# Optimization experiments

Measured on AMD Instinct MI355X. Metric: run time of the kernel, lower is better.

The kernel has to match this reference:

```python
import jax, jax.numpy as jnp
import numpy as np

N_NODES = 50000
N_EDGES = 800000
IN_CH = 128
HID = 256
N_GRAPHS = 512


def setup_inputs() -> dict:
    key = jax.random.key(0)
    ks = jax.random.split(key, 10)
    x = jax.random.normal(ks[0], (N_NODES, IN_CH), dtype=jnp.float32)
    edge_index = jax.random.randint(ks[1], (2, N_EDGES), 0, N_NODES, dtype=jnp.int32)
    batch = jnp.sort(jax.random.randint(ks[2], (N_NODES,), 0, N_GRAPHS, dtype=jnp.int32))
    # GCNConv params (glorot-ish init)
    W0 = jax.random.normal(ks[3], (IN_CH, HID), dtype=jnp.float32) / np.sqrt(IN_CH)
    b0 = jnp.zeros((HID,), dtype=jnp.float32)
    W1 = jax.random.normal(ks[4], (HID, HID), dtype=jnp.float32) / np.sqrt(HID)
    b1 = jnp.zeros((HID,), dtype=jnp.float32)
    W2 = jax.random.normal(ks[5], (HID, HID), dtype=jnp.float32) / np.sqrt(HID)
    b2 = jnp.zeros((HID,), dtype=jnp.float32)
    return {"x": x, "W0": W0, "b0": b0, "W1": W1, "b1": b1, "W2": W2, "b2": b2,
            "edge_index": edge_index, "batch": batch}


def _gcn_norm(edge_index, num_nodes):
    # PyG gcn_norm with add_self_loops=True: A_hat = A + I, norm = D^-1/2 A_hat D^-1/2
    src, dst = edge_index[0], edge_index[1]
    loop = jnp.arange(num_nodes, dtype=src.dtype)
    src = jnp.concatenate([src, loop])
    dst = jnp.concatenate([dst, loop])
    deg = jax.ops.segment_sum(jnp.ones_like(dst, dtype=jnp.float32), dst,
                              num_segments=num_nodes)
    dinv = jnp.where(deg > 0, jax.lax.rsqrt(deg), 0.0)
    norm = dinv[src] * dinv[dst]  # [E + N]
    return src, dst, norm


def _gcn_conv(x, W, b, src, dst, norm, num_nodes):
    h = x @ W                                  # [N, out]
    msg = norm[:, None] * h[src]               # gather + scale, [E+N, out]
    out = jax.ops.segment_sum(msg, dst, num_segments=num_nodes)  # scatter-add
    return out + b


def reference(x, W0, b0, W1, b1, W2, b2, edge_index, batch):
    n = x.shape[0]
    src, dst, norm = _gcn_norm(edge_index, n)  # normalization is layer-independent
    h = jax.nn.relu(_gcn_conv(x, W0, b0, src, dst, norm, n))
    h = jax.nn.relu(_gcn_conv(h, W1, b1, src, dst, norm, n))
    h = jax.nn.relu(_gcn_conv(h, W2, b2, src, dst, norm, n))
    # global_add_pool: segment-sum node features by graph id
    return jax.ops.segment_sum(h, batch, num_segments=N_GRAPHS)
```

## Files before the change

### kernel.cpp

```cpp
#include <hip/hip_runtime.h>
#include <hip/hip_fp16.h>

constexpr int NN  = 50000;
constexpr int NE  = 800000;
constexpr int CIN = 128;
constexpr int CH  = 256;
constexpr int NG  = 512;

typedef unsigned short ushort_t;
typedef unsigned int uint_t;
typedef unsigned char uchar_t;
typedef __attribute__((ext_vector_type(2))) float f32x2_t;
typedef __attribute__((ext_vector_type(2))) uint_t u32x2_t;

static __device__ __forceinline__ ushort_t f2bf(float f) {
    uint_t u = __float_as_uint(f);
    u += 0x7fffu + ((u >> 16) & 1u);
    return (ushort_t)(u >> 16);
}

static __device__ __forceinline__ float h16tof(uint_t bits) {
    return __half2float(__ushort_as_half((unsigned short)bits));
}

__global__ void conv_x_kernel(const float4* __restrict__ x, ushort4* __restrict__ xb, int n4) {
    int i = blockIdx.x * blockDim.x + threadIdx.x;
    if (i >= n4) return;
    float4 v = x[i];
    ushort4 o;
    o.x = f2bf(v.x); o.y = f2bf(v.y); o.z = f2bf(v.z); o.w = f2bf(v.w);
    xb[i] = o;
}

__global__ void conv_wt3_kernel(const float* __restrict__ W0, const float* __restrict__ W1,
                                const float* __restrict__ W2, ushort_t* __restrict__ W0t,
                                ushort_t* __restrict__ W1t, ushort_t* __restrict__ W2t) {
    int i = blockIdx.x * blockDim.x + threadIdx.x;
    if (i < 32768) {
        int k = i >> 8, n = i & 255;
        W0t[n * 128 + k] = f2bf(W0[i]);
    } else if (i < 98304) {
        int j = i - 32768;
        int k = j >> 8, n = j & 255;
        W1t[n * 256 + k] = f2bf(W1[j]);
    } else if (i < 163840) {
        int j = i - 98304;
        int k = j >> 8, n = j & 255;
        W2t[n * 256 + k] = f2bf(W2[j]);
    }
}

__global__ void count_kernel(const int* __restrict__ dst, int* __restrict__ cnt, int E) {
    int e = blockIdx.x * blockDim.x + threadIdx.x;
    if (e < E) atomicAdd(&cnt[dst[e]], 1);
}

__global__ __launch_bounds__(256) void scan_bsum_kernel(const int* __restrict__ cnt,
                                                        int* __restrict__ bsum, int n) {
    int i = blockIdx.x * 256 + threadIdx.x;
    int v = (i < n) ? ((cnt[i] + 7) & ~7) : 0;
    #pragma unroll
    for (int off = 32; off >= 1; off >>= 1) v += __shfl_xor(v, off, 64);
    __shared__ int ws[4];
    if ((threadIdx.x & 63) == 0) ws[threadIdx.x >> 6] = v;
    __syncthreads();
    if (threadIdx.x == 0) bsum[blockIdx.x] = ws[0] + ws[1] + ws[2] + ws[3];
}

__global__ __launch_bounds__(256) void scan_boff_kernel(int* __restrict__ bsum, int nb) {
    int tid = threadIdx.x, lane = tid & 63, wid = tid >> 6;
    int v = (tid < nb) ? bsum[tid] : 0;
    int s = v;
    #pragma unroll
    for (int off = 1; off < 64; off <<= 1) {
        int t = __shfl_up(s, off, 64);
        if (lane >= off) s += t;
    }
    __shared__ int wsum[4];
    if (lane == 63) wsum[wid] = s;
    __syncthreads();
    int wadd = 0;
    #pragma unroll
    for (int w = 0; w < 4; w++) if (w < wid) wadd += wsum[w];
    if (tid < nb) bsum[tid] = wadd + s - v;
}

__global__ __launch_bounds__(256) void scan_final_kernel(const int* __restrict__ cnt,
                                                         const int* __restrict__ boff,
                                                         int* __restrict__ rowptr,
                                                         float* __restrict__ dinv, int n) {
    int tid = threadIdx.x, lane = tid & 63, wid = tid >> 6;
    int i = blockIdx.x * 256 + tid;
    int c = (i < n) ? cnt[i] : 0;
    int v = (c + 7) & ~7;
    int s = v;
    #pragma unroll
    for (int off = 1; off < 64; off <<= 1) {
        int t = __shfl_up(s, off, 64);
        if (lane >= off) s += t;
    }
    __shared__ int wsum[4];
    if (lane == 63) wsum[wid] = s;
    __syncthreads();
    int wadd = boff[blockIdx.x];
    #pragma unroll
    for (int w = 0; w < 4; w++) if (w < wid) wadd += wsum[w];
    if (i < n) {
        rowptr[i] = wadd + s - v;
        dinv[i]   = rsqrtf((float)c + 1.0f);
        if (i == n - 1) rowptr[n] = wadd + s;
    }
}

__global__ void scatter_kernel(const int* __restrict__ src, const int* __restrict__ dst,
                               const int* __restrict__ rowptr, int* __restrict__ cursor,
                               const float* __restrict__ dinv, uint_t* __restrict__ epack, int E) {
    int e = blockIdx.x * blockDim.x + threadIdx.x;
    if (e >= E) return;
    int d = dst[e];
    int s = src[e];
    int p = rowptr[d] + atomicAdd(&cursor[d], 1);
    uint_t hb = (uint_t)__half_as_ushort(__float2half(dinv[s]));
    epack[p] = (uint_t)s | (hb << 16);
}

template <int C, int MODE>
__global__ __launch_bounds__(256) void node_agg_kernel(
    const ushort_t* __restrict__ h, const int* __restrict__ rowptr,
    const int* __restrict__ degc, const uint_t* __restrict__ epack,
    const float* __restrict__ dinv, const float* __restrict__ bias,
    const int* __restrict__ batch, void* __restrict__ out_v, int n) {
    constexpr int V = C / 64;
    int wave = threadIdx.x >> 6;
    int lane = threadIdx.x & 63;
    int d = blockIdx.x * 4 + wave;
    if (d >= n) return;

    int beg = __builtin_amdgcn_readfirstlane(rowptr[d]);
    int deg = __builtin_amdgcn_readfirstlane(degc[d]);
    const uint_t* hu = (const uint_t*)h;

    float acc[V] = {};
    const uint4* ep4 = (const uint4*)(epack + beg);
    uint4 ea, eb, na, nb;
    if (deg > 0) { ea = ep4[0]; eb = ep4[1]; }

    for (int e = 0; e < deg; e += 8) {
        int blk = e >> 3;
        if (e + 8 < deg) { na = ep4[blk * 2 + 2]; nb = ep4[blk * 2 + 3]; }
        uint_t eps[8] = {ea.x, ea.y, ea.z, ea.w, eb.x, eb.y, eb.z, eb.w};
        int   srcs[8];
        float wts[8];
        #pragma unroll
        for (int u = 0; u < 8; u++) {
            bool a = (e + u) < deg;
            srcs[u] = a ? (int)(eps[u] & 0xffffu) : d;
            wts[u]  = a ? h16tof(eps[u] >> 16) : 0.0f;
        }
        if constexpr (V == 4) {
            uint_t ra[8], rb[8];
            #pragma unroll
            for (int u = 0; u < 8; u++) {
                const uint_t* row = hu + (size_t)__builtin_amdgcn_readfirstlane(srcs[u]) * (C / 2);
                ra[u] = row[lane];
                rb[u] = row[64 + lane];
            }
            #pragma unroll
            for (int u = 0; u < 8; u++) {
                float w = wts[u];
                acc[0] += w * __uint_as_float(ra[u] << 16);
                acc[1] += w * __uint_as_float(ra[u] & 0xffff0000u);
                acc[2] += w * __uint_as_float(rb[u] << 16);
                acc[3] += w * __uint_as_float(rb[u] & 0xffff0000u);
            }
        } else {
            uint_t rv[8];
            #pragma unroll
            for (int u = 0; u < 8; u++) {
                const uint_t* row = hu + (size_t)__builtin_amdgcn_readfirstlane(srcs[u]) * (C / 2);
                rv[u] = row[lane];
            }
            #pragma unroll
            for (int u = 0; u < 8; u++) {
                float w = wts[u];
                acc[0] += w * __uint_as_float(rv[u] << 16);
                acc[1] += w * __uint_as_float(rv[u] & 0xffff0000u);
            }
        }
        ea = na; eb = nb;
    }

    float dd = dinv[d];
    float self[V];
    {
        const uint_t* row = hu + (size_t)d * (C / 2);
        uint_t sa = row[lane];
        self[0] = __uint_as_float(sa << 16);
        self[1] = __uint_as_float(sa & 0xffff0000u);
        if constexpr (V == 4) {
            uint_t sb = row[64 + lane];
            self[2] = __uint_as_float(sb << 16);
            self[3] = __uint_as_float(sb & 0xffff0000u);
        }
    }

    float r[V];
    if constexpr (MODE >= 1) {
        float2 bA = *(const float2*)(bias + 2 * lane);
        r[0] = fmaxf(dd * acc[0] + dd * dd * self[0] + bA.x, 0.0f);
        r[1] = fmaxf(dd * acc[1] + dd * dd * self[1] + bA.y, 0.0f);
        if constexpr (V == 4) {
            float2 bB = *(const float2*)(bias + 128 + 2 * lane);
            r[2] = fmaxf(dd * acc[2] + dd * dd * self[2] + bB.x, 0.0f);
            r[3] = fmaxf(dd * acc[3] + dd * dd * self[3] + bB.y, 0.0f);
        }
    } else {
        #pragma unroll
        for (int i = 0; i < V; i++)
            r[i] = dd * acc[i] + dd * dd * self[i];
    }

    if constexpr (MODE == 2) {
        float* o = (float*)out_v + (size_t)batch[d] * C;
        atomicAdd(o + 2 * lane, r[0]);
        atomicAdd(o + 2 * lane + 1, r[1]);
        if constexpr (V == 4) {
            atomicAdd(o + 128 + 2 * lane, r[2]);
            atomicAdd(o + 128 + 2 * lane + 1, r[3]);
        }
    } else {
        uint_t* o = (uint_t*)((ushort_t*)out_v + (size_t)d * C);
        __builtin_nontemporal_store((uint_t)f2bf(r[0]) | ((uint_t)f2bf(r[1]) << 16), &o[lane]);
        if constexpr (V == 4)
            __builtin_nontemporal_store((uint_t)f2bf(r[2]) | ((uint_t)f2bf(r[3]) << 16), &o[64 + lane]);
    }
}

template <int MODE>
__global__ __launch_bounds__(256) void node_agg_fp8_kernel(
    const uchar_t* __restrict__ h8, const int* __restrict__ rowptr,
    const int* __restrict__ degc, const uint_t* __restrict__ epack,
    const float* __restrict__ dinv, const float* __restrict__ bias,
    const int* __restrict__ batch, void* __restrict__ out_v, int n) {
    int wave = threadIdx.x >> 6;
    int lane = threadIdx.x & 63;
    int d = blockIdx.x * 4 + wave;
    if (d >= n) return;

    int beg = __builtin_amdgcn_readfirstlane(rowptr[d]);
    int deg = __builtin_amdgcn_readfirstlane(degc[d]);
    const uint_t* hu = (const uint_t*)h8;

    float a0 = 0.0f, a1 = 0.0f, a2 = 0.0f, a3 = 0.0f;
    const uint4* ep4 = (const uint4*)(epack + beg);
    uint4 ea, eb, na, nb;
    if (deg > 0) { ea = ep4[0]; eb = ep4[1]; }

    for (int e = 0; e < deg; e += 8) {
        int blk = e >> 3;
        if (e + 8 < deg) { na = ep4[blk * 2 + 2]; nb = ep4[blk * 2 + 3]; }
        uint_t eps[8] = {ea.x, ea.y, ea.z, ea.w, eb.x, eb.y, eb.z, eb.w};
        int   srcs[8];
        float wts[8];
        #pragma unroll
        for (int u = 0; u < 8; u++) {
            bool a = (e + u) < deg;
            srcs[u] = a ? (int)(eps[u] & 0xffffu) : d;
            wts[u]  = a ? h16tof(eps[u] >> 16) : 0.0f;
        }
        uint_t rv[8];
        #pragma unroll
        for (int u = 0; u < 8; u++)
            rv[u] = hu[(size_t)__builtin_amdgcn_readfirstlane(srcs[u]) * 64 + lane];
        #pragma unroll
        for (int u = 0; u < 8; u++) {
            float w = wts[u];
            f32x2_t lo = __builtin_amdgcn_cvt_pk_f32_fp8(rv[u], false);
            f32x2_t hi = __builtin_amdgcn_cvt_pk_f32_fp8(rv[u], true);
            a0 += w * lo.x;
            a1 += w * lo.y;
            a2 += w * hi.x;
            a3 += w * hi.y;
        }
        ea = na; eb = nb;
    }

    float dd = dinv[d];
    uint_t sv = hu[(size_t)d * 64 + lane];
    f32x2_t slo = __builtin_amdgcn_cvt_pk_f32_fp8(sv, false);
    f32x2_t shi = __builtin_amdgcn_cvt_pk_f32_fp8(sv, true);

    float4 b4 = *(const float4*)(bias + 4 * lane);
    float dd2 = dd * dd;
    float r0 = fmaxf(dd * a0 + dd2 * slo.x + b4.x, 0.0f);
    float r1 = fmaxf(dd * a1 + dd2 * slo.y + b4.y, 0.0f);
    float r2 = fmaxf(dd * a2 + dd2 * shi.x + b4.z, 0.0f);
    float r3 = fmaxf(dd * a3 + dd2 * shi.y + b4.w, 0.0f);

    if constexpr (MODE == 2) {
        float* o = (float*)out_v + (size_t)batch[d] * CH + 4 * lane;
        atomicAdd(o + 0, r0);
        atomicAdd(o + 1, r1);
        atomicAdd(o + 2, r2);
        atomicAdd(o + 3, r3);
    } else {
        u32x2_t st;
        st.x = (uint_t)f2bf(r0) | ((uint_t)f2bf(r1) << 16);
        st.y = (uint_t)f2bf(r2) | ((uint_t)f2bf(r3) << 16);
        u32x2_t* o = (u32x2_t*)((ushort_t*)out_v + (size_t)d * CH) + lane;
        __builtin_nontemporal_store(st, o);
    }
}

typedef __attribute__((ext_vector_type(8))) short bf16x8;
typedef __attribute__((ext_vector_type(4))) float f32x4;

template <int MODE, int F8OUT>
__global__ __launch_bounds__(256) void gemm_bf16_kernel(
    const ushort_t* __restrict__ A, const ushort_t* __restrict__ Wt,
    const float* __restrict__ bias, void* __restrict__ Cv, int M, int K) {
    __shared__ ushort_t As[128][40];
    __shared__ ushort_t Bs[128][40];
    int tid = threadIdx.x;
    int row0 = blockIdx.x * 128, col0 = blockIdx.y * 128;
    int lr = tid >> 2, lq = tid & 3;
    int lane = tid & 63, wv = tid >> 6;
    int wr = (wv >> 1) * 64, wc = (wv & 1) * 64;
    int r16 = lane & 15, quad = lane >> 4;

    f32x4 acc[4][4] = {};

    for (int k0 = 0; k0 < K; k0 += 32) {
        {
            int gr0 = row0 + lr, gr1 = row0 + lr + 64;
            uint4 a0 = make_uint4(0, 0, 0, 0), a1 = make_uint4(0, 0, 0, 0);
            if (gr0 < M) a0 = *(const uint4*)(A + (size_t)gr0 * K + k0 + lq * 8);
            if (gr1 < M) a1 = *(const uint4*)(A + (size_t)gr1 * K + k0 + lq * 8);
            *(uint4*)&As[lr][lq * 8]      = a0;
            *(uint4*)&As[lr + 64][lq * 8] = a1;
            uint4 b0 = *(const uint4*)(Wt + (size_t)(col0 + lr) * K + k0 + lq * 8);
            uint4 b1 = *(const uint4*)(Wt + (size_t)(col0 + lr + 64) * K + k0 + lq * 8);
            *(uint4*)&Bs[lr][lq * 8]      = b0;
            *(uint4*)&Bs[lr + 64][lq * 8] = b1;
        }
        __syncthreads();
        bf16x8 af[4], bfr[4];
        #pragma unroll
        for (int i = 0; i < 4; i++) af[i]  = *(const bf16x8*)&As[wr + i * 16 + r16][quad * 8];
        #pragma unroll
        for (int j = 0; j < 4; j++) bfr[j] = *(const bf16x8*)&Bs[wc + j * 16 + r16][quad * 8];
        #pragma unroll
        for (int i = 0; i < 4; i++)
            #pragma unroll
            for (int j = 0; j < 4; j++)
                acc[i][j] = __builtin_amdgcn_mfma_f32_16x16x32_bf16(af[i], bfr[j], acc[i][j], 0, 0, 0);
        __syncthreads();
    }

    #pragma unroll
    for (int j = 0; j < 4; j++) {
        int colc = col0 + wc + j * 16 + r16;
        float bval = (MODE == 1) ? bias[colc] : 0.0f;
        #pragma unroll
        for (int i = 0; i < 4; i++) {
            #pragma unroll
            for (int r = 0; r < 4; r++) {
                int row = row0 + wr + i * 16 + quad * 4 + r;
                if (row < M) {
                    float v = acc[i][j][r];
                    if (MODE == 1) v = fmaxf(v + bval, 0.0f);
                    if constexpr (F8OUT) {
                        uint_t pk = __builtin_amdgcn_cvt_pk_fp8_f32(v, v, 0u, false);
                        ((uchar_t*)Cv)[(size_t)row * 256 + colc] = (uchar_t)(pk & 0xffu);
                    } else {
                        ((ushort_t*)Cv)[(size_t)row * 256 + colc] = f2bf(v);
                    }
                }
            }
        }
    }
}

extern "C" void kernel_launch(void* const* d_in, const int* in_sizes, int n_in,
                              void* d_out, int out_size, void* d_ws, size_t ws_size,
                              hipStream_t stream) {
    const float* x   = (const float*)d_in[0];
    const float* W0  = (const float*)d_in[1];
    const float* b0  = (const float*)d_in[2];
    const float* W1  = (const float*)d_in[3];
    const float* b1  = (const float*)d_in[4];
    const float* W2  = (const float*)d_in[5];
    const float* b2  = (const float*)d_in[6];
    const int*   ei  = (const int*)d_in[7];
    const int*   src = ei;
    const int*   dst = ei + NE;
    const int*   batch = (const int*)d_in[8];
    float* out = (float*)d_out;

    char* ws = (char*)d_ws;
    ushort_t* P1  = (ushort_t*)ws;
    ushort_t* G0  = (ushort_t*)(ws + 25600000ull);
    uchar_t*  F8  = (uchar_t*) (ws + 38400000ull);
    ushort_t* xbf = (ushort_t*)(ws + 51200000ull);
    ushort_t* W0t = (ushort_t*)(ws + 64000000ull);
    ushort_t* W1t = (ushort_t*)(ws + 64065536ull);
    ushort_t* W2t = (ushort_t*)(ws + 64196608ull);
    float*    dinv   = (float*)(ws + 64327680ull);
    int*      rowptr = (int*)  (ws + 64527680ull);
    int*      cnt    = (int*)  (ws + 64727808ull);
    uint_t*   epack  = (uint_t*)(ws + 64927808ull);
    int*      bsum   = (int*)  (ws + 71327808ull);
    int*      cursor = (int*)ws;

    const int scanBlocks = (NN + 255) / 256;
    const int nodeBlocks = (NN + 3) / 4;
    const dim3 ggrid((NN + 127) / 128, 2);

    conv_x_kernel<<<(NN * CIN / 4 + 255) / 256, 256, 0, stream>>>((const float4*)x, (ushort4*)xbf, NN * CIN / 4);
    conv_wt3_kernel<<<640, 256, 0, stream>>>(W0, W1, W2, W0t, W1t, W2t);

    hipMemsetAsync(cnt, 0, (size_t)NN * 4, stream);
    count_kernel<<<(NE + 255) / 256, 256, 0, stream>>>(dst, cnt, NE);
    scan_bsum_kernel<<<scanBlocks, 256, 0, stream>>>(cnt, bsum, NN);
    scan_boff_kernel<<<1, 256, 0, stream>>>(bsum, scanBlocks);
    scan_final_kernel<<<scanBlocks, 256, 0, stream>>>(cnt, bsum, rowptr, dinv, NN);
    hipMemsetAsync(cursor, 0, (size_t)NN * 4, stream);
    scatter_kernel<<<(NE + 255) / 256, 256, 0, stream>>>(src, dst, rowptr, cursor, dinv, epack, NE);

    node_agg_kernel<CIN, 0><<<nodeBlocks, 256, 0, stream>>>(xbf, rowptr, cnt, epack, dinv, nullptr, nullptr, G0, NN);
    gemm_bf16_kernel<1, 0><<<ggrid, 256, 0, stream>>>(G0, W0t, b0, P1, NN, CIN);

    gemm_bf16_kernel<0, 1><<<ggrid, 256, 0, stream>>>(P1, W1t, nullptr, F8, NN, CH);
    node_agg_fp8_kernel<1><<<nodeBlocks, 256, 0, stream>>>(F8, rowptr, cnt, epack, dinv, b1, nullptr, P1, NN);

    gemm_bf16_kernel<0, 1><<<ggrid, 256, 0, stream>>>(P1, W2t, nullptr, F8, NN, CH);
    hipMemsetAsync(out, 0, (size_t)NG * CH * 4, stream);
    node_agg_fp8_kernel<2><<<nodeBlocks, 256, 0, stream>>>(F8, rowptr, cnt, epack, dinv, b2, batch, out, NN);
}
```

Before: 489.3 us.

## Stage fp8 GEMM output through LDS for coalesced stores; drop nontemporal stores

The fp8-output GEMM epilogue now writes converted bytes into a shared-memory tile that aliases the A/B staging buffers, then stores whole rows to global memory as 16-byte vectors instead of scattered single-byte writes. Nontemporal stores in the node-aggregation kernels are replaced with ordinary stores, so the bf16 outputs can stay in cache for the GEMM that reads them next. A READ2 variant of the fp8 aggregation, reading two 16-bit halves per lane with a matching output layout, is enabled only for the final pooling layer. The costs are an extra barrier and LDS round trip in the epilogue, plus narrower gathers in the last layer.

```diff
diff --git a/kernel.cpp b/kernel.cpp
--- a/kernel.cpp
+++ b/kernel.cpp
@@ -230,13 +230,13 @@
         }
     } else {
         uint_t* o = (uint_t*)((ushort_t*)out_v + (size_t)d * C);
-        __builtin_nontemporal_store((uint_t)f2bf(r[0]) | ((uint_t)f2bf(r[1]) << 16), &o[lane]);
+        o[lane] = (uint_t)f2bf(r[0]) | ((uint_t)f2bf(r[1]) << 16);
         if constexpr (V == 4)
-            __builtin_nontemporal_store((uint_t)f2bf(r[2]) | ((uint_t)f2bf(r[3]) << 16), &o[64 + lane]);
-    }
-}
-
-template <int MODE>
+            o[64 + lane] = (uint_t)f2bf(r[2]) | ((uint_t)f2bf(r[3]) << 16);
+    }
+}
+
+template <int MODE, int READ2>
 __global__ __launch_bounds__(256) void node_agg_fp8_kernel(
     const uchar_t* __restrict__ h8, const int* __restrict__ rowptr,
     const int* __restrict__ degc, const uint_t* __restrict__ epack,
@@ -249,7 +249,6 @@
 
     int beg = __builtin_amdgcn_readfirstlane(rowptr[d]);
     int deg = __builtin_amdgcn_readfirstlane(degc[d]);
-    const uint_t* hu = (const uint_t*)h8;
 
     float a0 = 0.0f, a1 = 0.0f, a2 = 0.0f, a3 = 0.0f;
     const uint4* ep4 = (const uint4*)(epack + beg);
@@ -268,47 +267,90 @@
             srcs[u] = a ? (int)(eps[u] & 0xffffu) : d;
             wts[u]  = a ? h16tof(eps[u] >> 16) : 0.0f;
         }
-        uint_t rv[8];
-        #pragma unroll
-        for (int u = 0; u < 8; u++)
-            rv[u] = hu[(size_t)__builtin_amdgcn_readfirstlane(srcs[u]) * 64 + lane];
-        #pragma unroll
-        for (int u = 0; u < 8; u++) {
-            float w = wts[u];
-            f32x2_t lo = __builtin_amdgcn_cvt_pk_f32_fp8(rv[u], false);
-            f32x2_t hi = __builtin_amdgcn_cvt_pk_f32_fp8(rv[u], true);
-            a0 += w * lo.x;
-            a1 += w * lo.y;
-            a2 += w * hi.x;
-            a3 += w * hi.y;
+        if constexpr (READ2) {
+            uint_t ra[8], rb[8];
+            #pragma unroll
+            for (int u = 0; u < 8; u++) {
+                const ushort_t* row = (const ushort_t*)h8 + (size_t)__builtin_amdgcn_readfirstlane(srcs[u]) * 128;
+                ra[u] = row[lane];
+                rb[u] = row[64 + lane];
+            }
+            #pragma unroll
+            for (int u = 0; u < 8; u++) {
+                float w = wts[u];
+                f32x2_t lo = __builtin_amdgcn_cvt_pk_f32_fp8(ra[u], false);
+                f32x2_t hi = __builtin_amdgcn_cvt_pk_f32_fp8(rb[u], false);
+                a0 += w * lo.x;
+                a1 += w * lo.y;
+                a2 += w * hi.x;
+                a3 += w * hi.y;
+            }
+        } else {
+            const uint_t* hu = (const uint_t*)h8;
+            uint_t rv[8];
+            #pragma unroll
+            for (int u = 0; u < 8; u++)
+                rv[u] = hu[(size_t)__builtin_amdgcn_readfirstlane(srcs[u]) * 64 + lane];
+            #pragma unroll
+            for (int u = 0; u < 8; u++) {
+                float w = wts[u];
+                f32x2_t lo = __builtin_amdgcn_cvt_pk_f32_fp8(rv[u], false);
+                f32x2_t hi = __builtin_amdgcn_cvt_pk_f32_fp8(rv[u], true);
+                a0 += w * lo.x;
+                a1 += w * lo.y;
+                a2 += w * hi.x;
+                a3 += w * hi.y;
+            }
         }
         ea = na; eb = nb;
     }
 
     float dd = dinv[d];
-    uint_t sv = hu[(size_t)d * 64 + lane];
-    f32x2_t slo = __builtin_amdgcn_cvt_pk_f32_fp8(sv, false);
-    f32x2_t shi = __builtin_amdgcn_cvt_pk_f32_fp8(sv, true);
-
-    float4 b4 = *(const float4*)(bias + 4 * lane);
     float dd2 = dd * dd;
-    float r0 = fmaxf(dd * a0 + dd2 * slo.x + b4.x, 0.0f);
-    float r1 = fmaxf(dd * a1 + dd2 * slo.y + b4.y, 0.0f);
-    float r2 = fmaxf(dd * a2 + dd2 * shi.x + b4.z, 0.0f);
-    float r3 = fmaxf(dd * a3 + dd2 * shi.y + b4.w, 0.0f);
-
-    if constexpr (MODE == 2) {
-        float* o = (float*)out_v + (size_t)batch[d] * CH + 4 * lane;
-        atomicAdd(o + 0, r0);
-        atomicAdd(o + 1, r1);
-        atomicAdd(o + 2, r2);
-        atomicAdd(o + 3, r3);
+
+    if constexpr (READ2) {
+        const ushort_t* srow = (const ushort_t*)h8 + (size_t)d * 128;
+        f32x2_t slo = __builtin_amdgcn_cvt_pk_f32_fp8((uint_t)srow[lane], false);
+        f32x2_t shi = __builtin_amdgcn_cvt_pk_f32_fp8((uint_t)srow[64 + lane], false);
+        float2 bA = *(const float2*)(bias + 2 * lane);
+        float2 bB = *(const float2*)(bias + 128 + 2 * lane);
+        float r0 = fmaxf(dd * a0 + dd2 * slo.x + bA.x, 0.0f);
+        float r1 = fmaxf(dd * a1 + dd2 * slo.y + bA.y, 0.0f);
+        float r2 = fmaxf(dd * a2 + dd2 * shi.x + bB.x, 0.0f);
+        float r3 = fmaxf(dd * a3 + dd2 * shi.y + bB.y, 0.0f);
+        if constexpr (MODE == 2) {
+            float* o = (float*)out_v + (size_t)batch[d] * CH;
+            atomicAdd(o + 2 * lane, r0);
+            atomicAdd(o + 2 * lane + 1, r1);
+            atomicAdd(o + 128 + 2 * lane, r2);
+            atomicAdd(o + 128 + 2 * lane + 1, r3);
+        } else {
+            uint_t* o = (uint_t*)((ushort_t*)out_v + (size_t)d * CH);
+            o[lane]      = (uint_t)f2bf(r0) | ((uint_t)f2bf(r1) << 16);
+            o[64 + lane] = (uint_t)f2bf(r2) | ((uint_t)f2bf(r3) << 16);
+        }
     } else {
-        u32x2_t st;
-        st.x = (uint_t)f2bf(r0) | ((uint_t)f2bf(r1) << 16);
-        st.y = (uint_t)f2bf(r2) | ((uint_t)f2bf(r3) << 16);
-        u32x2_t* o = (u32x2_t*)((ushort_t*)out_v + (size_t)d * CH) + lane;
-        __builtin_nontemporal_store(st, o);
+        const uint_t* hu = (const uint_t*)h8;
+        uint_t sv = hu[(size_t)d * 64 + lane];
+        f32x2_t slo = __builtin_amdgcn_cvt_pk_f32_fp8(sv, false);
+        f32x2_t shi = __builtin_amdgcn_cvt_pk_f32_fp8(sv, true);
+        float4 b4 = *(const float4*)(bias + 4 * lane);
+        float r0 = fmaxf(dd * a0 + dd2 * slo.x + b4.x, 0.0f);
+        float r1 = fmaxf(dd * a1 + dd2 * slo.y + b4.y, 0.0f);
+        float r2 = fmaxf(dd * a2 + dd2 * shi.x + b4.z, 0.0f);
+        float r3 = fmaxf(dd * a3 + dd2 * shi.y + b4.w, 0.0f);
+        if constexpr (MODE == 2) {
+            float* o = (float*)out_v + (size_t)batch[d] * CH + 4 * lane;
+            atomicAdd(o + 0, r0);
+            atomicAdd(o + 1, r1);
+            atomicAdd(o + 2, r2);
+            atomicAdd(o + 3, r3);
+        } else {
+            u32x2_t st;
+            st.x = (uint_t)f2bf(r0) | ((uint_t)f2bf(r1) << 16);
+            st.y = (uint_t)f2bf(r2) | ((uint_t)f2bf(r3) << 16);
+            *((u32x2_t*)((ushort_t*)out_v + (size_t)d * CH) + lane) = st;
+        }
     }
 }
 
@@ -319,8 +361,10 @@
 __global__ __launch_bounds__(256) void gemm_bf16_kernel(
     const ushort_t* __restrict__ A, const ushort_t* __restrict__ Wt,
     const float* __restrict__ bias, void* __restrict__ Cv, int M, int K) {
-    __shared__ ushort_t As[128][40];
-    __shared__ ushort_t Bs[128][40];
+    __shared__ union alignas(16) {
+        ushort_t ab[2][128][40];
+        uchar_t  f8[128][128];
+    } smem;
     int tid = threadIdx.x;
     int row0 = blockIdx.x * 128, col0 = blockIdx.y * 128;
     int lr = tid >> 2, lq = tid & 3;
@@ -336,19 +380,19 @@
             uint4 a0 = make_uint4(0, 0, 0, 0), a1 = make_uint4(0, 0, 0, 0);
             if (gr0 < M) a0 = *(const uint4*)(A + (size_t)gr0 * K + k0 + lq * 8);
             if (gr1 < M) a1 = *(const uint4*)(A + (size_t)gr1 * K + k0 + lq * 8);
-            *(uint4*)&As[lr][lq * 8]      = a0;
-            *(uint4*)&As[lr + 64][lq * 8] = a1;
+            *(uint4*)&smem.ab[0][lr][lq * 8]      = a0;
+            *(uint4*)&smem.ab[0][lr + 64][lq * 8] = a1;
             uint4 b0 = *(const uint4*)(Wt + (size_t)(col0 + lr) * K + k0 + lq * 8);
             uint4 b1 = *(const uint4*)(Wt + (size_t)(col0 + lr + 64) * K + k0 + lq * 8);
-            *(uint4*)&Bs[lr][lq * 8]      = b0;
-            *(uint4*)&Bs[lr + 64][lq * 8] = b1;
+            *(uint4*)&smem.ab[1][lr][lq * 8]      = b0;
+            *(uint4*)&smem.ab[1][lr + 64][lq * 8] = b1;
         }
         __syncthreads();
         bf16x8 af[4], bfr[4];
         #pragma unroll
-        for (int i = 0; i < 4; i++) af[i]  = *(const bf16x8*)&As[wr + i * 16 + r16][quad * 8];
-        #pragma unroll
-        for (int j = 0; j < 4; j++) bfr[j] = *(const bf16x8*)&Bs[wc + j * 16 + r16][quad * 8];
+        for (int i = 0; i < 4; i++) af[i]  = *(const bf16x8*)&smem.ab[0][wr + i * 16 + r16][quad * 8];
+        #pragma unroll
+        for (int j = 0; j < 4; j++) bfr[j] = *(const bf16x8*)&smem.ab[1][wc + j * 16 + r16][quad * 8];
         #pragma unroll
         for (int i = 0; i < 4; i++)
             #pragma unroll
@@ -357,22 +401,43 @@
         __syncthreads();
     }
 
-    #pragma unroll
-    for (int j = 0; j < 4; j++) {
-        int colc = col0 + wc + j * 16 + r16;
-        float bval = (MODE == 1) ? bias[colc] : 0.0f;
-        #pragma unroll
-        for (int i = 0; i < 4; i++) {
-            #pragma unroll
-            for (int r = 0; r < 4; r++) {
-                int row = row0 + wr + i * 16 + quad * 4 + r;
-                if (row < M) {
+    if constexpr (F8OUT) {
+        #pragma unroll
+        for (int j = 0; j < 4; j++) {
+            int colt = wc + j * 16 + r16;
+            #pragma unroll
+            for (int i = 0; i < 4; i++) {
+                #pragma unroll
+                for (int r = 0; r < 4; r++) {
                     float v = acc[i][j][r];
-                    if (MODE == 1) v = fmaxf(v + bval, 0.0f);
-                    if constexpr (F8OUT) {
-                        uint_t pk = __builtin_amdgcn_cvt_pk_fp8_f32(v, v, 0u, false);
-                        ((uchar_t*)Cv)[(size_t)row * 256 + colc] = (uchar_t)(pk & 0xffu);
-                    } else {
+                    uint_t pk = __builtin_amdgcn_cvt_pk_fp8_f32(v, v, 0u, false);
+                    smem.f8[wr + i * 16 + quad * 4 + r][colt] = (uchar_t)(pk & 0xffu);
+                }
+            }
+        }
+        __syncthreads();
+        uchar_t* C8 = (uchar_t*)Cv;
+        #pragma unroll
+        for (int k = 0; k < 4; k++) {
+            int idx = k * 256 + tid;
+            int r = idx >> 3, coff = (idx & 7) * 16;
+            if (row0 + r < M)
+                *(uint4*)(C8 + (size_t)(row0 + r) * 256 + col0 + coff) =
+                    *(const uint4*)&smem.f8[r][coff];
+        }
+    } else {
+        #pragma unroll
+        for (int j = 0; j < 4; j++) {
+            int colc = col0 + wc + j * 16 + r16;
+            float bval = (MODE == 1) ? bias[colc] : 0.0f;
+            #pragma unroll
+            for (int i = 0; i < 4; i++) {
+                #pragma unroll
+                for (int r = 0; r < 4; r++) {
+                    int row = row0 + wr + i * 16 + quad * 4 + r;
+                    if (row < M) {
+                        float v = acc[i][j][r];
+                        if (MODE == 1) v = fmaxf(v + bval, 0.0f);
                         ((ushort_t*)Cv)[(size_t)row * 256 + colc] = f2bf(v);
                     }
                 }
@@ -431,9 +496,9 @@
     gemm_bf16_kernel<1, 0><<<ggrid, 256, 0, stream>>>(G0, W0t, b0, P1, NN, CIN);
 
     gemm_bf16_kernel<0, 1><<<ggrid, 256, 0, stream>>>(P1, W1t, nullptr, F8, NN, CH);
-    node_agg_fp8_kernel<1><<<nodeBlocks, 256, 0, stream>>>(F8, rowptr, cnt, epack, dinv, b1, nullptr, P1, NN);
+    node_agg_fp8_kernel<1, 0><<<nodeBlocks, 256, 0, stream>>>(F8, rowptr, cnt, epack, dinv, b1, nullptr, P1, NN);
 
     gemm_bf16_kernel<0, 1><<<ggrid, 256, 0, stream>>>(P1, W2t, nullptr, F8, NN, CH);
     hipMemsetAsync(out, 0, (size_t)NG * CH * 4, stream);
-    node_agg_fp8_kernel<2><<<nodeBlocks, 256, 0, stream>>>(F8, rowptr, cnt, epack, dinv, b2, batch, out, NN);
-}
+    node_agg_fp8_kernel<2, 1><<<nodeBlocks, 256, 0, stream>>>(F8, rowptr, cnt, epack, dinv, b2, batch, out, NN);
+}
```

Measured after the change: 397.3 us. 18.8% less time.

## Widen edge batches to 16 and stage FP8 GEMM output through LDS

Applied to the files above, without the earlier changes.

Row padding in the CSR grows from 8 to 16 edges, and both aggregation kernels now handle 16 neighbor gathers per iteration. This puts more independent loads in flight to hide gather latency. The FP8 GEMM epilogue now writes its tile into shared memory and then stores 16-byte coalesced rows, replacing the scattered single-byte global stores. Nontemporal stores become plain stores and the first-layer aggregation becomes a dedicated 128-channel kernel. The trade-offs are higher register pressure, more padded edge slots to load, and an extra barrier in the GEMM.

```diff
diff --git a/kernel.cpp b/kernel.cpp
--- a/kernel.cpp
+++ b/kernel.cpp
@@ -58,7 +58,7 @@
 __global__ __launch_bounds__(256) void scan_bsum_kernel(const int* __restrict__ cnt,
                                                         int* __restrict__ bsum, int n) {
     int i = blockIdx.x * 256 + threadIdx.x;
-    int v = (i < n) ? ((cnt[i] + 7) & ~7) : 0;
+    int v = (i < n) ? ((cnt[i] + 15) & ~15) : 0;
     #pragma unroll
     for (int off = 32; off >= 1; off >>= 1) v += __shfl_xor(v, off, 64);
     __shared__ int ws[4];
@@ -92,7 +92,7 @@
     int tid = threadIdx.x, lane = tid & 63, wid = tid >> 6;
     int i = blockIdx.x * 256 + tid;
     int c = (i < n) ? cnt[i] : 0;
-    int v = (c + 7) & ~7;
+    int v = (c + 15) & ~15;
     int s = v;
     #pragma unroll
     for (int off = 1; off < 64; off <<= 1) {
@@ -124,13 +124,10 @@
     epack[p] = (uint_t)s | (hb << 16);
 }
 
-template <int C, int MODE>
-__global__ __launch_bounds__(256) void node_agg_kernel(
+__global__ __launch_bounds__(256) void node_agg_bf16_kernel(
     const ushort_t* __restrict__ h, const int* __restrict__ rowptr,
     const int* __restrict__ degc, const uint_t* __restrict__ epack,
-    const float* __restrict__ dinv, const float* __restrict__ bias,
-    const int* __restrict__ batch, void* __restrict__ out_v, int n) {
-    constexpr int V = C / 64;
+    const float* __restrict__ dinv, ushort_t* __restrict__ outp, int n) {
     int wave = threadIdx.x >> 6;
     int lane = threadIdx.x & 63;
     int d = blockIdx.x * 4 + wave;
@@ -140,100 +137,48 @@
     int deg = __builtin_amdgcn_readfirstlane(degc[d]);
     const uint_t* hu = (const uint_t*)h;
 
-    float acc[V] = {};
+    float a0 = 0.0f, a1 = 0.0f;
     const uint4* ep4 = (const uint4*)(epack + beg);
-    uint4 ea, eb, na, nb;
-    if (deg > 0) { ea = ep4[0]; eb = ep4[1]; }
-
-    for (int e = 0; e < deg; e += 8) {
-        int blk = e >> 3;
-        if (e + 8 < deg) { na = ep4[blk * 2 + 2]; nb = ep4[blk * 2 + 3]; }
-        uint_t eps[8] = {ea.x, ea.y, ea.z, ea.w, eb.x, eb.y, eb.z, eb.w};
-        int   srcs[8];
-        float wts[8];
-        #pragma unroll
-        for (int u = 0; u < 8; u++) {
+    uint4 e0, e1, e2, e3;
+    if (deg > 0) { e0 = ep4[0]; e1 = ep4[1]; e2 = ep4[2]; e3 = ep4[3]; }
+    uint4 n0 = e0, n1 = e1, n2 = e2, n3 = e3;
+
+    for (int e = 0; e < deg; e += 16) {
+        int blk = e >> 4;
+        if (e + 16 < deg) {
+            n0 = ep4[blk * 4 + 4]; n1 = ep4[blk * 4 + 5];
+            n2 = ep4[blk * 4 + 6]; n3 = ep4[blk * 4 + 7];
+        }
+        uint_t eps[16] = {e0.x, e0.y, e0.z, e0.w, e1.x, e1.y, e1.z, e1.w,
+                          e2.x, e2.y, e2.z, e2.w, e3.x, e3.y, e3.z, e3.w};
+        int   srcs[16];
+        float wts[16];
+        #pragma unroll
+        for (int u = 0; u < 16; u++) {
             bool a = (e + u) < deg;
             srcs[u] = a ? (int)(eps[u] & 0xffffu) : d;
             wts[u]  = a ? h16tof(eps[u] >> 16) : 0.0f;
         }
-        if constexpr (V == 4) {
-            uint_t ra[8], rb[8];
-            #pragma unroll
-            for (int u = 0; u < 8; u++) {
-                const uint_t* row = hu + (size_t)__builtin_amdgcn_readfirstlane(srcs[u]) * (C / 2);
-                ra[u] = row[lane];
-                rb[u] = row[64 + lane];
-            }
-            #pragma unroll
-            for (int u = 0; u < 8; u++) {
-                float w = wts[u];
-                acc[0] += w * __uint_as_float(ra[u] << 16);
-                acc[1] += w * __uint_as_float(ra[u] & 0xffff0000u);
-                acc[2] += w * __uint_as_float(rb[u] << 16);
-                acc[3] += w * __uint_as_float(rb[u] & 0xffff0000u);
-            }
-        } else {
-            uint_t rv[8];
-            #pragma unroll
-            for (int u = 0; u < 8; u++) {
-                const uint_t* row = hu + (size_t)__builtin_amdgcn_readfirstlane(srcs[u]) * (C / 2);
-                rv[u] = row[lane];
-            }
-            #pragma unroll
-            for (int u = 0; u < 8; u++) {
-                float w = wts[u];
-                acc[0] += w * __uint_as_float(rv[u] << 16);
-                acc[1] += w * __uint_as_float(rv[u] & 0xffff0000u);
-            }
-        }
-        ea = na; eb = nb;
+        uint_t rv[16];
+        #pragma unroll
+        for (int u = 0; u < 16; u++)
+            rv[u] = hu[(size_t)__builtin_amdgcn_readfirstlane(srcs[u]) * 64 + lane];
+        #pragma unroll
+        for (int u = 0; u < 16; u++) {
+            float w = wts[u];
+            a0 += w * __uint_as_float(rv[u] << 16);
+            a1 += w * __uint_as_float(rv[u] & 0xffff0000u);
+        }
+        e0 = n0; e1 = n1; e2 = n2; e3 = n3;
     }
 
     float dd = dinv[d];
-    float self[V];
-    {
-        const uint_t* row = hu + (size_t)d * (C / 2);
-        uint_t sa = row[lane];
-        self[0] = __uint_as_float(sa << 16);
-        self[1] = __uint_as_float(sa & 0xffff0000u);
-        if constexpr (V == 4) {
-            uint_t sb = row[64 + lane];
-            self[2] = __uint_as_float(sb << 16);
-            self[3] = __uint_as_float(sb & 0xffff0000u);
-        }
-    }
-
-    float r[V];
-    if constexpr (MODE >= 1) {
-        float2 bA = *(const float2*)(bias + 2 * lane);
-        r[0] = fmaxf(dd * acc[0] + dd * dd * self[0] + bA.x, 0.0f);
-        r[1] = fmaxf(dd * acc[1] + dd * dd * self[1] + bA.y, 0.0f);
-        if constexpr (V == 4) {
-            float2 bB = *(const float2*)(bias + 128 + 2 * lane);
-            r[2] = fmaxf(dd * acc[2] + dd * dd * self[2] + bB.x, 0.0f);
-            r[3] = fmaxf(dd * acc[3] + dd * dd * self[3] + bB.y, 0.0f);
-        }
-    } else {
-        #pragma unroll
-        for (int i = 0; i < V; i++)
-            r[i] = dd * acc[i] + dd * dd * self[i];
-    }
-
-    if constexpr (MODE == 2) {
-        float* o = (float*)out_v + (size_t)batch[d] * C;
-        atomicAdd(o + 2 * lane, r[0]);
-        atomicAdd(o + 2 * lane + 1, r[1]);
-        if constexpr (V == 4) {
-            atomicAdd(o + 128 + 2 * lane, r[2]);
-            atomicAdd(o + 128 + 2 * lane + 1, r[3]);
-        }
-    } else {
-        uint_t* o = (uint_t*)((ushort_t*)out_v + (size_t)d * C);
-        __builtin_nontemporal_store((uint_t)f2bf(r[0]) | ((uint_t)f2bf(r[1]) << 16), &o[lane]);
-        if constexpr (V == 4)
-            __builtin_nontemporal_store((uint_t)f2bf(r[2]) | ((uint_t)f2bf(r[3]) << 16), &o[64 + lane]);
-    }
+    uint_t sv = hu[(size_t)d * 64 + lane];
+    float r0 = dd * a0 + dd * dd * __uint_as_float(sv << 16);
+    float r1 = dd * a1 + dd * dd * __uint_as_float(sv & 0xffff0000u);
+
+    uint_t* o = (uint_t*)(outp + (size_t)d * CIN);
+    o[lane] = (uint_t)f2bf(r0) | ((uint_t)f2bf(r1) << 16);
 }
 
 template <int MODE>
@@ -253,27 +198,32 @@
 
     float a0 = 0.0f, a1 = 0.0f, a2 = 0.0f, a3 = 0.0f;
     const uint4* ep4 = (const uint4*)(epack + beg);
-    uint4 ea, eb, na, nb;
-    if (deg > 0) { ea = ep4[0]; eb = ep4[1]; }
-
-    for (int e = 0; e < deg; e += 8) {
-        int blk = e >> 3;
-        if (e + 8 < deg) { na = ep4[blk * 2 + 2]; nb = ep4[blk * 2 + 3]; }
-        uint_t eps[8] = {ea.x, ea.y, ea.z, ea.w, eb.x, eb.y, eb.z, eb.w};
-        int   srcs[8];
-        float wts[8];
-        #pragma unroll
-        for (int u = 0; u < 8; u++) {
+    uint4 e0, e1, e2, e3;
+    if (deg > 0) { e0 = ep4[0]; e1 = ep4[1]; e2 = ep4[2]; e3 = ep4[3]; }
+    uint4 n0 = e0, n1 = e1, n2 = e2, n3 = e3;
+
+    for (int e = 0; e < deg; e += 16) {
+        int blk = e >> 4;
+        if (e + 16 < deg) {
+            n0 = ep4[blk * 4 + 4]; n1 = ep4[blk * 4 + 5];
+            n2 = ep4[blk * 4 + 6]; n3 = ep4[blk * 4 + 7];
+        }
+        uint_t eps[16] = {e0.x, e0.y, e0.z, e0.w, e1.x, e1.y, e1.z, e1.w,
+                          e2.x, e2.y, e2.z, e2.w, e3.x, e3.y, e3.z, e3.w};
+        int   srcs[16];
+        float wts[16];
+        #pragma unroll
+        for (int u = 0; u < 16; u++) {
             bool a = (e + u) < deg;
             srcs[u] = a ? (int)(eps[u] & 0xffffu) : d;
             wts[u]  = a ? h16tof(eps[u] >> 16) : 0.0f;
         }
-        uint_t rv[8];
-        #pragma unroll
-        for (int u = 0; u < 8; u++)
+        uint_t rv[16];
+        #pragma unroll
+        for (int u = 0; u < 16; u++)
             rv[u] = hu[(size_t)__builtin_amdgcn_readfirstlane(srcs[u]) * 64 + lane];
         #pragma unroll
-        for (int u = 0; u < 8; u++) {
+        for (int u = 0; u < 16; u++) {
             float w = wts[u];
             f32x2_t lo = __builtin_amdgcn_cvt_pk_f32_fp8(rv[u], false);
             f32x2_t hi = __builtin_amdgcn_cvt_pk_f32_fp8(rv[u], true);
@@ -282,16 +232,16 @@
             a2 += w * hi.x;
             a3 += w * hi.y;
         }
-        ea = na; eb = nb;
+        e0 = n0; e1 = n1; e2 = n2; e3 = n3;
     }
 
     float dd = dinv[d];
+    float dd2 = dd * dd;
     uint_t sv = hu[(size_t)d * 64 + lane];
     f32x2_t slo = __builtin_amdgcn_cvt_pk_f32_fp8(sv, false);
     f32x2_t shi = __builtin_amdgcn_cvt_pk_f32_fp8(sv, true);
 
     float4 b4 = *(const float4*)(bias + 4 * lane);
-    float dd2 = dd * dd;
     float r0 = fmaxf(dd * a0 + dd2 * slo.x + b4.x, 0.0f);
     float r1 = fmaxf(dd * a1 + dd2 * slo.y + b4.y, 0.0f);
     float r2 = fmaxf(dd * a2 + dd2 * shi.x + b4.z, 0.0f);
@@ -307,8 +257,7 @@
         u32x2_t st;
         st.x = (uint_t)f2bf(r0) | ((uint_t)f2bf(r1) << 16);
         st.y = (uint_t)f2bf(r2) | ((uint_t)f2bf(r3) << 16);
-        u32x2_t* o = (u32x2_t*)((ushort_t*)out_v + (size_t)d * CH) + lane;
-        __builtin_nontemporal_store(st, o);
+        *((u32x2_t*)((ushort_t*)out_v + (size_t)d * CH) + lane) = st;
     }
 }
 
@@ -319,8 +268,10 @@
 __global__ __launch_bounds__(256) void gemm_bf16_kernel(
     const ushort_t* __restrict__ A, const ushort_t* __restrict__ Wt,
     const float* __restrict__ bias, void* __restrict__ Cv, int M, int K) {
-    __shared__ ushort_t As[128][40];
-    __shared__ ushort_t Bs[128][40];
+    __shared__ union alignas(16) {
+        ushort_t ab[2][128][40];
+        uchar_t  f8[128][128];
+    } smem;
     int tid = threadIdx.x;
     int row0 = blockIdx.x * 128, col0 = blockIdx.y * 128;
     int lr = tid >> 2, lq = tid & 3;
@@ -336,19 +287,19 @@
             uint4 a0 = make_uint4(0, 0, 0, 0), a1 = make_uint4(0, 0, 0, 0);
             if (gr0 < M) a0 = *(const uint4*)(A + (size_t)gr0 * K + k0 + lq * 8);
             if (gr1 < M) a1 = *(const uint4*)(A + (size_t)gr1 * K + k0 + lq * 8);
-            *(uint4*)&As[lr][lq * 8]      = a0;
-            *(uint4*)&As[lr + 64][lq * 8] = a1;
+            *(uint4*)&smem.ab[0][lr][lq * 8]      = a0;
+            *(uint4*)&smem.ab[0][lr + 64][lq * 8] = a1;
             uint4 b0 = *(const uint4*)(Wt + (size_t)(col0 + lr) * K + k0 + lq * 8);
             uint4 b1 = *(const uint4*)(Wt + (size_t)(col0 + lr + 64) * K + k0 + lq * 8);
-            *(uint4*)&Bs[lr][lq * 8]      = b0;
-            *(uint4*)&Bs[lr + 64][lq * 8] = b1;
+            *(uint4*)&smem.ab[1][lr][lq * 8]      = b0;
+            *(uint4*)&smem.ab[1][lr + 64][lq * 8] = b1;
         }
         __syncthreads();
         bf16x8 af[4], bfr[4];
         #pragma unroll
-        for (int i = 0; i < 4; i++) af[i]  = *(const bf16x8*)&As[wr + i * 16 + r16][quad * 8];
-        #pragma unroll
-        for (int j = 0; j < 4; j++) bfr[j] = *(const bf16x8*)&Bs[wc + j * 16 + r16][quad * 8];
+        for (int i = 0; i < 4; i++) af[i]  = *(const bf16x8*)&smem.ab[0][wr + i * 16 + r16][quad * 8];
+        #pragma unroll
+        for (int j = 0; j < 4; j++) bfr[j] = *(const bf16x8*)&smem.ab[1][wc + j * 16 + r16][quad * 8];
         #pragma unroll
         for (int i = 0; i < 4; i++)
             #pragma unroll
@@ -357,22 +308,43 @@
         __syncthreads();
     }
 
-    #pragma unroll
-    for (int j = 0; j < 4; j++) {
-        int colc = col0 + wc + j * 16 + r16;
-        float bval = (MODE == 1) ? bias[colc] : 0.0f;
-        #pragma unroll
-        for (int i = 0; i < 4; i++) {
+    if constexpr (F8OUT) {
+        #pragma unroll
+        for (int j = 0; j < 4; j++) {
+            int colt = wc + j * 16 + r16;
             #pragma unroll
-            for (int r = 0; r < 4; r++) {
-                int row = row0 + wr + i * 16 + quad * 4 + r;
-                if (row < M) {
+            for (int i = 0; i < 4; i++) {
+                #pragma unroll
+                for (int r = 0; r < 4; r++) {
                     float v = acc[i][j][r];
-                    if (MODE == 1) v = fmaxf(v + bval, 0.0f);
-                    if constexpr (F8OUT) {
-                        uint_t pk = __builtin_amdgcn_cvt_pk_fp8_f32(v, v, 0u, false);
-                        ((uchar_t*)Cv)[(size_t)row * 256 + colc] = (uchar_t)(pk & 0xffu);
-                    } else {
+                    uint_t pk = __builtin_amdgcn_cvt_pk_fp8_f32(v, v, 0u, false);
+                    smem.f8[wr + i * 16 + quad * 4 + r][colt] = (uchar_t)(pk & 0xffu);
+                }
+            }
+        }
+        __syncthreads();
+        uchar_t* C8 = (uchar_t*)Cv;
+        #pragma unroll
+        for (int k = 0; k < 4; k++) {
+            int idx = k * 256 + tid;
+            int r = idx >> 3, coff = (idx & 7) * 16;
+            if (row0 + r < M)
+                *(uint4*)(C8 + (size_t)(row0 + r) * 256 + col0 + coff) =
+                    *(const uint4*)&smem.f8[r][coff];
+        }
+    } else {
+        #pragma unroll
+        for (int j = 0; j < 4; j++) {
+            int colc = col0 + wc + j * 16 + r16;
+            float bval = (MODE == 1) ? bias[colc] : 0.0f;
+            #pragma unroll
+            for (int i = 0; i < 4; i++) {
+                #pragma unroll
+                for (int r = 0; r < 4; r++) {
+                    int row = row0 + wr + i * 16 + quad * 4 + r;
+                    if (row < M) {
+                        float v = acc[i][j][r];
+                        if (MODE == 1) v = fmaxf(v + bval, 0.0f);
                         ((ushort_t*)Cv)[(size_t)row * 256 + colc] = f2bf(v);
                     }
                 }
@@ -427,7 +399,7 @@
     hipMemsetAsync(cursor, 0, (size_t)NN * 4, stream);
     scatter_kernel<<<(NE + 255) / 256, 256, 0, stream>>>(src, dst, rowptr, cursor, dinv, epack, NE);
 
-    node_agg_kernel<CIN, 0><<<nodeBlocks, 256, 0, stream>>>(xbf, rowptr, cnt, epack, dinv, nullptr, nullptr, G0, NN);
+    node_agg_bf16_kernel<<<nodeBlocks, 256, 0, stream>>>(xbf, rowptr, cnt, epack, dinv, G0, NN);
     gemm_bf16_kernel<1, 0><<<ggrid, 256, 0, stream>>>(G0, W0t, b0, P1, NN, CIN);
 
     gemm_bf16_kernel<0, 1><<<ggrid, 256, 0, stream>>>(P1, W1t, nullptr, F8, NN, CH);
```

New measurement: 492.4 us. No clear change (+0.6%).
